# Optimization experiments

Hardware: AMD Instinct MI355X
Metric: run time of the kernel (lower is better)

## Reference

```python
import jax, jax.numpy as jnp
import numpy as np

R = 32          # grid_resolution
C_DIM = 128
HID = 128
N_BLOCKS = 5
PAD = 0.1
N_FREQ = 10

def setup_inputs() -> dict:
    key = jax.random.key(0)
    ks = jax.random.split(key, 10)
    B, T = 4, 65536
    s = 0.05
    return {
        "p": jax.random.uniform(ks[0], (B, T, 3), jnp.float32, -0.5, 0.5),
        "fc_pos_w": jax.random.normal(ks[1], (60, 2 * HID), jnp.float32) * s,
        "fc_pos_b": jax.random.normal(ks[2], (2 * HID,), jnp.float32) * s,
        "fc0_w": jax.random.normal(ks[3], (N_BLOCKS, 2 * HID, HID), jnp.float32) * s,
        "fc0_b": jax.random.normal(ks[4], (N_BLOCKS, HID), jnp.float32) * s,
        "fc1_w": jax.random.normal(ks[5], (N_BLOCKS, HID, HID), jnp.float32) * s,
        "fc1_b": jax.random.normal(ks[6], (N_BLOCKS, HID), jnp.float32) * s,
        "sc_w": jax.random.normal(ks[7], (N_BLOCKS, 2 * HID, HID), jnp.float32) * s,
        "fc_c_w": jax.random.normal(ks[8], (HID, C_DIM), jnp.float32) * s,
        "fc_c_b": jax.random.normal(ks[9], (C_DIM,), jnp.float32) * s,
    }

def _pos_enc(p):
    # NeRF-style: per frequency append sin then cos -> [B,T,3*2*10]=60
    freqs = (2.0 ** jnp.arange(N_FREQ, dtype=p.dtype)) * np.pi
    outs = []
    for i in range(N_FREQ):
        outs.append(jnp.sin(freqs[i] * p))
        outs.append(jnp.cos(freqs[i] * p))
    return jnp.concatenate(outs, axis=-1)

def _grid_index(p):
    # normalize_3d_coordinate + coordinate2index (3d)
    p_nor = p / (1.0 + PAD + 1e-3) + 0.5
    p_nor = jnp.clip(p_nor, 0.0, 1.0 - 1e-3)
    xi = (p_nor * R).astype(jnp.int32)
    return xi[..., 0] + R * (xi[..., 1] + R * xi[..., 2])  # [B,T]

def _resblock(x, w0, b0, w1, b1, ws):
    # ResnetBlockFC: fc_0(relu(x)) -> fc_1(relu(net)); shortcut Linear(no bias)
    net = jnp.maximum(x, 0) @ w0 + b0
    dx = jnp.maximum(net, 0) @ w1 + b1
    return x @ ws + dx

def _seg_max(c, idx):  # c [T,D], idx [T]
    return jax.ops.segment_max(c, idx, num_segments=R ** 3)

def _seg_sum(c, idx):
    return jax.ops.segment_sum(c, idx, num_segments=R ** 3)

def reference(p, fc_pos_w, fc_pos_b, fc0_w, fc0_b, fc1_w, fc1_b, sc_w, fc_c_w, fc_c_b):
    B = p.shape[0]
    index = _grid_index(p)                               # [B,T] int32
    net = _pos_enc(p) @ fc_pos_w + fc_pos_b              # [B,T,256]
    net = _resblock(net, fc0_w[0], fc0_b[0], fc1_w[0], fc1_b[0], sc_w[0])  # [B,T,128]
    for i in range(1, N_BLOCKS):
        # pool_local: scatter_max per voxel, gather back at each point
        fea = jax.vmap(_seg_max)(net, index)             # [B,R^3,128]
        pooled = jnp.take_along_axis(fea, index[..., None], axis=1)  # [B,T,128]
        net = jnp.concatenate([net, pooled], axis=-1)    # [B,T,256]
        net = _resblock(net, fc0_w[i], fc0_b[i], fc1_w[i], fc1_b[i], sc_w[i])
    c = net @ fc_c_w + fc_c_b                            # [B,T,128]
    # generate_grid_features: scatter_mean into R^3 voxels (empty voxels -> 0)
    sums = jax.vmap(_seg_sum)(c, index)                  # [B,R^3,128]
    cnt = jax.vmap(_seg_sum)(jnp.ones(index.shape + (1,), c.dtype), index)
    mean = sums / jnp.maximum(cnt, 1.0)
    fea_grid = mean.transpose(0, 2, 1).reshape(B, C_DIM, R, R, R)
    return fea_grid
```

## Files before the change

kernel.cpp:

```cpp
#include <hip/hip_runtime.h>

typedef _Float16 hf;
typedef _Float16 hf8 __attribute__((ext_vector_type(8)));
typedef float f32x4 __attribute__((ext_vector_type(4)));

static constexpr int BATCH = 4;
static constexpr int TPTS  = 65536;
static constexpr int NPTS  = BATCH * TPTS;
static constexpr int R3    = 32768;
static constexpr int NVOX  = BATCH * R3;

static constexpr int OFF_WPOS = 0;
static constexpr int OFF_W0   = 16384;
static constexpr int OFF_W1   = 180224;
static constexpr int OFF_WSC  = 262144;
static constexpr int OFF_WC   = 425984;
static constexpr int NCHUNKS  = 55296;

__device__ constexpr int kpat(int g, int j) { return (j & 3) + 4 * g + 16 * (j >> 2); }

#define MFMA16(a, b, c) __builtin_amdgcn_mfma_f32_16x16x32_f16((a), (b), (c), 0, 0, 0)

__device__ inline hf8 relu8(hf8 a) {
#pragma unroll
  for (int i = 0; i < 8; ++i) a[i] = (a[i] > (hf)0) ? a[i] : (hf)0;
  return a;
}
__device__ inline f32x4 splat4(float v) {
  f32x4 r; r[0] = v; r[1] = v; r[2] = v; r[3] = v; return r;
}
__device__ inline hf8 ldfrag(const hf* __restrict__ base, int kc, int nt, int NT, int lane) {
  return *(const hf8*)(base + (((size_t)(kc * NT + nt) * 64 + lane) << 3));
}

__global__ __launch_bounds__(256) void k_prep(
    const float* __restrict__ wpos, const float* __restrict__ w0,
    const float* __restrict__ w1,  const float* __restrict__ wsc,
    const float* __restrict__ wc,  hf* __restrict__ fr)
{
  const int cid = blockIdx.x * 256 + threadIdx.x;
  if (cid >= NCHUNKS) return;
  const float* src; hf* dst; int NT, N, kmax, loc;
  if (cid < 2048) {
    src = wpos; dst = fr + OFF_WPOS; NT = 16; N = 256; kmax = 60; loc = cid;
  } else if (cid < 22528) {
    int l5 = cid - 2048; int i = l5 >> 12; loc = l5 & 4095;
    src = w0 + (size_t)i * 32768; dst = fr + OFF_W0 + (size_t)i * 32768;
    NT = 8; N = 128; kmax = 256;
  } else if (cid < 32768) {
    int l5 = cid - 22528; int i = l5 >> 11; loc = l5 & 2047;
    src = w1 + (size_t)i * 16384; dst = fr + OFF_W1 + (size_t)i * 16384;
    NT = 8; N = 128; kmax = 128;
  } else if (cid < 53248) {
    int l5 = cid - 32768; int i = l5 >> 12; loc = l5 & 4095;
    src = wsc + (size_t)i * 32768; dst = fr + OFF_WSC + (size_t)i * 32768;
    NT = 8; N = 128; kmax = 256;
  } else {
    loc = cid - 53248; src = wc; dst = fr + OFF_WC; NT = 8; N = 128; kmax = 128;
  }
  const int lane = loc & 63;
  const int rest = loc >> 6;
  const int nt = rest % NT, kc = rest / NT;
  const int g = lane >> 4;
  const int n = nt * 16 + (lane & 15);
  union { hf8 h; hf f[8]; } o;
#pragma unroll
  for (int j = 0; j < 8; ++j) {
    int k = kc * 32 + kpat(g, j);
    o.f[j] = (k < kmax) ? (hf)src[(size_t)k * N + n] : (hf)0;
  }
  *(hf8*)(dst + ((size_t)loc << 3)) = o.h;
}

__global__ __launch_bounds__(256) void k_idxcnt(
    const float* __restrict__ p, int* __restrict__ idxbuf, int* __restrict__ cnt)
{
  const int t = blockIdx.x * 256 + threadIdx.x;
  const float px = p[(size_t)t * 3 + 0];
  const float py = p[(size_t)t * 3 + 1];
  const float pz = p[(size_t)t * 3 + 2];
  float nx = fminf(fmaxf(px / 1.101f + 0.5f, 0.0f), 0.999f);
  float ny = fminf(fmaxf(py / 1.101f + 0.5f, 0.0f), 0.999f);
  float nz = fminf(fmaxf(pz / 1.101f + 0.5f, 0.0f), 0.999f);
  const int iv = (int)(nx * 32.f) + 32 * (int)(ny * 32.f) + 1024 * (int)(nz * 32.f);
  idxbuf[t] = iv;
  atomicAdd(&cnt[((t >> 16) << 15) | iv], 1);
}

__global__ __launch_bounds__(256) void k_scan(
    const int* __restrict__ cnt, int* __restrict__ start, int* __restrict__ total)
{
  __shared__ int s[256];
  __shared__ int base_s;
  const int tid = threadIdx.x;
  const int v0 = blockIdx.x * 512;
  const int a = cnt[v0 + 2 * tid], b = cnt[v0 + 2 * tid + 1];
  const int sum = a + b;
  s[tid] = sum;
  __syncthreads();
  for (int off = 1; off < 256; off <<= 1) {
    int x = (tid >= off) ? s[tid - off] : 0;
    __syncthreads();
    s[tid] += x;
    __syncthreads();
  }
  if (tid == 255) base_s = atomicAdd(total, s[255]);
  __syncthreads();
  const int excl = base_s + s[tid] - sum;
  start[v0 + 2 * tid]     = excl;
  start[v0 + 2 * tid + 1] = excl + a;
}

__global__ __launch_bounds__(256) void k_fill(
    int* __restrict__ idxbuf, int* __restrict__ start, int* __restrict__ svox)
{
  const int t = blockIdx.x * 256 + threadIdx.x;
  const int bv = ((t >> 16) << 15) | idxbuf[t];
  const int pos = atomicAdd(&start[bv], 1);
  svox[pos] = bv;
  idxbuf[t] = pos;
}

__global__ __launch_bounds__(256, 4) void k_fused0(
    const float* __restrict__ p, const hf* __restrict__ fr,
    const float* __restrict__ bpos,
    const hf* __restrict__ w0f, const hf* __restrict__ w1f,
    const hf* __restrict__ wscf,
    const float* __restrict__ b0, const float* __restrict__ b1,
    const int* __restrict__ spos, hf* __restrict__ net)
{
  __shared__ __align__(16) hf swX[16384];
  __shared__ int sp[64];
  const int tid = threadIdx.x;
  const int wv = tid >> 6, lane = tid & 63;
  const int r = lane & 15, g = lane >> 4;
  const int t0 = blockIdx.x * 64;

  if (tid < 64) sp[tid] = spos[t0 + tid];

  if (tid < 64) {
    const int mt = tid >> 4, rr = tid & 15;
    *(unsigned long long*)(swX + (((mt * 2 + 1) * 64 + 48 + rr) << 3) + 4) = 0ull;
  }
#pragma unroll
  for (int i = 0; i < 8; ++i) {
    const int tau = tid + i * 256;
    if (tau >= 1920) break;
    const int pt = (int)(((unsigned)tau * 34953u) >> 20);
    const int a  = tau - pt * 30;
    const int fi = (a * 11) >> 5;
    const int comp = a - 3 * fi;
    const float pc = p[(size_t)(t0 + pt) * 3 + comp];
    const float ang = (float)(1 << fi) * 3.14159274101257324f * pc;
    const float sv = __sinf(ang), cv = __cosf(ang);
    const int mt = pt >> 4, rr = pt & 15;
    const int ks = 6 * fi + comp;
    {
      const int kc = ks >> 5, kk = ks & 31, gg = (kk >> 2) & 3;
      const int e = (kk & 3) + 4 * (kk >> 4);
      swX[(((mt * 2 + kc) * 64 + gg * 16 + rr) << 3) + e] = (hf)sv;
    }
    {
      const int kco = ks + 3;
      const int kc = kco >> 5, kk = kco & 31, gg = (kk >> 2) & 3;
      const int e = (kk & 3) + 4 * (kk >> 4);
      swX[(((mt * 2 + kc) * 64 + gg * 16 + rr) << 3) + e] = (hf)cv;
    }
  }
  __syncthreads();

  f32x4 acc[4][4];
#pragma unroll
  for (int nf = 0; nf < 4; ++nf) {
    float bv = bpos[wv * 64 + nf * 16 + r];
#pragma unroll
    for (int mf = 0; mf < 4; ++mf) acc[mf][nf] = splat4(bv);
  }
#pragma unroll
  for (int kc = 0; kc < 2; ++kc) {
    hf8 a[4];
#pragma unroll
    for (int mf = 0; mf < 4; ++mf)
      a[mf] = *(const hf8*)(swX + (((mf * 2 + kc) * 64 + lane) << 3));
#pragma unroll
    for (int nf = 0; nf < 4; ++nf) {
      hf8 b = ldfrag(fr + OFF_WPOS, kc, wv * 4 + nf, 16, lane);
#pragma unroll
      for (int mf = 0; mf < 4; ++mf) acc[mf][nf] = MFMA16(a[mf], b, acc[mf][nf]);
    }
  }
  __syncthreads();

#pragma unroll
  for (int mf = 0; mf < 4; ++mf)
#pragma unroll
    for (int nf = 0; nf < 4; ++nf)
#pragma unroll
      for (int reg = 0; reg < 4; ++reg) {
        int rr = 4 * g + reg;
        int c  = wv * 64 + nf * 16 + r;
        int kc = c >> 5;
        int kk = c & 31;
        int gg = (kk >> 2) & 3;
        int e  = (kk & 3) + 4 * (kk >> 4);
        int slot = gg * 16 + ((rr + gg) & 15);
        swX[(((size_t)(mf * 8 + kc) * 64 + slot) << 3) + e] = (hf)acc[mf][nf][reg];
      }
  __syncthreads();

  const int wm = wv >> 1, wn = wv & 1;
  const int lidx = g * 16 + ((r + g) & 15);

  f32x4 h[2][4], d[2][4];
#pragma unroll
  for (int nf = 0; nf < 4; ++nf) {
    const int n = wn * 64 + nf * 16 + r;
    const float bh = b0[n], bd = b1[n];
#pragma unroll
    for (int mf = 0; mf < 2; ++mf) { h[mf][nf] = splat4(bh); d[mf][nf] = splat4(bd); }
  }
#pragma unroll 2
  for (int kc = 0; kc < 8; ++kc) {
    hf8 a[2], ar[2];
#pragma unroll
    for (int mf = 0; mf < 2; ++mf) {
      a[mf] = *(const hf8*)(swX + (((size_t)((wm * 2 + mf) * 8 + kc) * 64 + lidx) << 3));
      ar[mf] = relu8(a[mf]);
    }
#pragma unroll
    for (int nf = 0; nf < 4; ++nf) {
      hf8 bw0 = ldfrag(w0f, kc, wn * 4 + nf, 8, lane);
      hf8 bws = ldfrag(wscf, kc, wn * 4 + nf, 8, lane);
#pragma unroll
      for (int mf = 0; mf < 2; ++mf) {
        h[mf][nf] = MFMA16(ar[mf], bw0, h[mf][nf]);
        d[mf][nf] = MFMA16(a[mf],  bws, d[mf][nf]);
      }
    }
  }
  __syncthreads();

#pragma unroll
  for (int mf = 0; mf < 2; ++mf)
#pragma unroll
    for (int nf = 0; nf < 4; ++nf)
#pragma unroll
      for (int reg = 0; reg < 4; ++reg) {
        int m = wm * 32 + mf * 16 + 4 * g + reg;
        int k = wn * 64 + nf * 16 + r;
        float hv = fmaxf(h[mf][nf][reg], 0.f);
        int mt = m >> 4, rr = m & 15;
        int kc = k >> 5, kk = k & 31;
        int gg = (kk >> 2) & 3;
        int e = (kk & 3) + 4 * (kk >> 4);
        int slot = gg * 16 + ((rr + gg) & 15);
        swX[(((size_t)(mt * 4 + kc) * 64 + slot) << 3) + e] = (hf)hv;
      }
  __syncthreads();

#pragma unroll
  for (int kc = 0; kc < 4; ++kc) {
    hf8 a[2];
#pragma unroll
    for (int mf = 0; mf < 2; ++mf)
      a[mf] = *(const hf8*)(swX + (((size_t)((wm * 2 + mf) * 4 + kc) * 64 + lidx) << 3));
#pragma unroll
    for (int nf = 0; nf < 4; ++nf) {
      hf8 bw1 = ldfrag(w1f, kc, wn * 4 + nf, 8, lane);
#pragma unroll
      for (int mf = 0; mf < 2; ++mf) d[mf][nf] = MFMA16(a[mf], bw1, d[mf][nf]);
    }
  }

#pragma unroll
  for (int mf = 0; mf < 2; ++mf)
#pragma unroll
    for (int nf = 0; nf < 4; ++nf)
#pragma unroll
      for (int reg = 0; reg < 4; ++reg) {
        int m = wm * 32 + mf * 16 + 4 * g + reg;
        int n = wn * 64 + nf * 16 + r;
        net[(size_t)sp[m] * 128 + n] = (hf)d[mf][nf][reg];
      }
}

__global__ __launch_bounds__(256) void k_pool(
    const hf* __restrict__ net, const int* __restrict__ svox,
    hf* __restrict__ fea)
{
  const int tid = threadIdx.x;
  const int grp = tid >> 4, q = tid & 15;
  const int gbeg = blockIdx.x * 128 + grp * 8;
  const int gend = gbeg + 8;
  int i = gbeg;
  while (i < gend) {
    const int v = svox[i];
    if (i != 0 && svox[i - 1] == v) { ++i; continue; }
    float m[8];
#pragma unroll
    for (int e = 0; e < 8; ++e) m[e] = -1e30f;
    int j = i;
    do {
      union { uint4 u; hf h[8]; } x;
      x.u = *(const uint4*)(net + (size_t)j * 128 + 8 * q);
#pragma unroll
      for (int e = 0; e < 8; ++e) m[e] = fmaxf(m[e], (float)x.h[e]);
      ++j;
    } while (j < NPTS && svox[j] == v);
    union { uint4 u; hf h[8]; } o;
#pragma unroll
    for (int e = 0; e < 8; ++e) o.h[e] = (hf)m[e];
    *(uint4*)(fea + ((size_t)v << 7) + 8 * q) = o.u;
    i = j;
  }
}

template <int LAST>
__global__ __launch_bounds__(256, 2) void k_res(
    hf* __restrict__ net, const hf* __restrict__ fea,
    const int* __restrict__ svox,
    const hf* __restrict__ w0f, const hf* __restrict__ w1f,
    const hf* __restrict__ wscf,
    const float* __restrict__ b0, const float* __restrict__ b1,
    const hf* __restrict__ wcf, const float* __restrict__ bc)
{
  __shared__ __align__(16) hf swX[32768];
  const int tid = threadIdx.x;
  const int wv = tid >> 6, lane = tid & 63;
  const int r = lane & 15, g = lane >> 4;
  const int wm = wv >> 1, wn = wv & 1;
  const int t0 = blockIdx.x * 128;
  const int lidx = g * 16 + ((r + g) & 15);

  for (int cc = tid; cc < 4096; cc += 256) {
    const int cl = cc & 63;
    const int kc = (cc >> 6) & 7;
    const int mt = cc >> 9;
    const int rr = cl & 15, gg = cl >> 4;
    const int t = t0 + mt * 16 + rr;
    const int c1 = kc * 32 + 4 * gg;
    union { hf8 h; uint2 u2[2]; } x;
    const hf* srcp;
    if (kc < 4) {
      srcp = net + (size_t)t * 128 + c1;
    } else {
      srcp = fea + (((size_t)svox[t]) << 7) + (c1 - 128);
    }
    x.u2[0] = *(const uint2*)(srcp);
    x.u2[1] = *(const uint2*)(srcp + 16);
    const int slot = gg * 16 + ((rr + gg) & 15);
    *(hf8*)(swX + (((size_t)((cc & ~63) + slot)) << 3)) = x.h;
  }
  __syncthreads();

  f32x4 h[4][4], d[4][4];
#pragma unroll
  for (int nf = 0; nf < 4; ++nf) {
    const int n = wn * 64 + nf * 16 + r;
    const float bh = b0[n], bd = b1[n];
#pragma unroll
    for (int mf = 0; mf < 4; ++mf) { h[mf][nf] = splat4(bh); d[mf][nf] = splat4(bd); }
  }
#pragma unroll 2
  for (int kc = 0; kc < 8; ++kc) {
    hf8 a[4], ar[4];
#pragma unroll
    for (int mf = 0; mf < 4; ++mf) {
      a[mf] = *(const hf8*)(swX + (((size_t)((wm * 4 + mf) * 8 + kc) * 64 + lidx) << 3));
      ar[mf] = relu8(a[mf]);
    }
#pragma unroll
    for (int nf = 0; nf < 4; ++nf) {
      hf8 bw0 = ldfrag(w0f, kc, wn * 4 + nf, 8, lane);
      hf8 bws = ldfrag(wscf, kc, wn * 4 + nf, 8, lane);
#pragma unroll
      for (int mf = 0; mf < 4; ++mf) {
        h[mf][nf] = MFMA16(ar[mf], bw0, h[mf][nf]);
        d[mf][nf] = MFMA16(a[mf],  bws, d[mf][nf]);
      }
    }
  }
  __syncthreads();

#pragma unroll
  for (int mf = 0; mf < 4; ++mf)
#pragma unroll
    for (int nf = 0; nf < 4; ++nf)
#pragma unroll
      for (int reg = 0; reg < 4; ++reg) {
        int m = wm * 64 + mf * 16 + 4 * g + reg;
        int k = wn * 64 + nf * 16 + r;
        float hv = fmaxf(h[mf][nf][reg], 0.f);
        int mt = m >> 4, rr = m & 15;
        int kc = k >> 5, kk = k & 31;
        int gg = (kk >> 2) & 3;
        int e = (kk & 3) + 4 * (kk >> 4);
        int slot = gg * 16 + ((rr + gg) & 15);
        swX[(((size_t)(mt * 4 + kc) * 64 + slot) << 3) + e] = (hf)hv;
      }
  __syncthreads();

#pragma unroll
  for (int kc = 0; kc < 4; ++kc) {
    hf8 a[4];
#pragma unroll
    for (int mf = 0; mf < 4; ++mf)
      a[mf] = *(const hf8*)(swX + (((size_t)((wm * 4 + mf) * 4 + kc) * 64 + lidx) << 3));
#pragma unroll
    for (int nf = 0; nf < 4; ++nf) {
      hf8 bw1 = ldfrag(w1f, kc, wn * 4 + nf, 8, lane);
#pragma unroll
      for (int mf = 0; mf < 4; ++mf) d[mf][nf] = MFMA16(a[mf], bw1, d[mf][nf]);
    }
  }

  if (LAST) {
    __syncthreads();
#pragma unroll
    for (int mf = 0; mf < 4; ++mf)
#pragma unroll
      for (int nf = 0; nf < 4; ++nf)
#pragma unroll
        for (int reg = 0; reg < 4; ++reg) {
          int m = wm * 64 + mf * 16 + 4 * g + reg;
          int k = wn * 64 + nf * 16 + r;
          int mt = m >> 4, rr = m & 15;
          int kc = k >> 5, kk = k & 31;
          int gg = (kk >> 2) & 3;
          int e = (kk & 3) + 4 * (kk >> 4);
          int slot = gg * 16 + ((rr + gg) & 15);
          swX[(((size_t)(mt * 4 + kc) * 64 + slot) << 3) + e] = (hf)d[mf][nf][reg];
        }
    __syncthreads();

    f32x4 c2[4][4];
#pragma unroll
    for (int nf = 0; nf < 4; ++nf) {
      float bv = bc[wn * 64 + nf * 16 + r];
#pragma unroll
      for (int mf = 0; mf < 4; ++mf) c2[mf][nf] = splat4(bv);
    }
#pragma unroll
    for (int kc = 0; kc < 4; ++kc) {
      hf8 a[4];
#pragma unroll
      for (int mf = 0; mf < 4; ++mf)
        a[mf] = *(const hf8*)(swX + (((size_t)((wm * 4 + mf) * 4 + kc) * 64 + lidx) << 3));
#pragma unroll
      for (int nf = 0; nf < 4; ++nf) {
        hf8 bw = ldfrag(wcf, kc, wn * 4 + nf, 8, lane);
#pragma unroll
        for (int mf = 0; mf < 4; ++mf) c2[mf][nf] = MFMA16(a[mf], bw, c2[mf][nf]);
      }
    }
#pragma unroll
    for (int mf = 0; mf < 4; ++mf)
#pragma unroll
      for (int nf = 0; nf < 4; ++nf)
#pragma unroll
        for (int reg = 0; reg < 4; ++reg) {
          int m = wm * 64 + mf * 16 + 4 * g + reg;
          int n = wn * 64 + nf * 16 + r;
          net[(size_t)(t0 + m) * 128 + n] = (hf)c2[mf][nf][reg];
        }
  } else {
#pragma unroll
    for (int mf = 0; mf < 4; ++mf)
#pragma unroll
      for (int nf = 0; nf < 4; ++nf)
#pragma unroll
        for (int reg = 0; reg < 4; ++reg) {
          int m = wm * 64 + mf * 16 + 4 * g + reg;
          int n = wn * 64 + nf * 16 + r;
          net[(size_t)(t0 + m) * 128 + n] = (hf)d[mf][nf][reg];
        }
  }
}

__global__ __launch_bounds__(256) void k_write(
    const hf* __restrict__ cbuf, const int* __restrict__ start,
    const int* __restrict__ cnt, float* __restrict__ out)
{
  __shared__ float tile[128 * 65];
  const int tid = threadIdx.x;
  const int grp = tid >> 4, q = tid & 15;
  const int g0 = blockIdx.x * 64;
  for (int vl = grp; vl < 64; vl += 16) {
    const int bv = g0 + vl;
    const int n = cnt[bv];
    const int end = start[bv], beg = end - n;
    float s[8] = {0, 0, 0, 0, 0, 0, 0, 0};
    for (int i = beg; i < end; ++i) {
      union { uint4 u; hf h[8]; } x;
      x.u = *(const uint4*)(cbuf + (size_t)i * 128 + 8 * q);
#pragma unroll
      for (int e = 0; e < 8; ++e) s[e] += (float)x.h[e];
    }
    const float inv = 1.0f / fmaxf((float)n, 1.0f);
#pragma unroll
    for (int e = 0; e < 8; ++e) tile[(8 * q + e) * 65 + vl] = s[e] * inv;
  }
  __syncthreads();
  const int b = g0 >> 15, v0 = g0 & 32767;
  for (int i = tid; i < 8192; i += 256) {
    const int c = i >> 6, vl = i & 63;
    out[(((size_t)(b * 128 + c)) << 15) + v0 + vl] = tile[c * 65 + vl];
  }
}

extern "C" void kernel_launch(void* const* d_in, const int* in_sizes, int n_in,
                              void* d_out, int out_size, void* d_ws, size_t ws_size,
                              hipStream_t stream)
{
  const float* p    = (const float*)d_in[0];
  const float* wpos = (const float*)d_in[1];
  const float* bpos = (const float*)d_in[2];
  const float* w0   = (const float*)d_in[3];
  const float* b0   = (const float*)d_in[4];
  const float* w1   = (const float*)d_in[5];
  const float* b1   = (const float*)d_in[6];
  const float* wsc  = (const float*)d_in[7];
  const float* wc   = (const float*)d_in[8];
  const float* bc   = (const float*)d_in[9];

  char* ws = (char*)d_ws;
  int* idxbuf = (int*)ws;
  hf*  net    = (hf*)(ws + (1u << 20));
  hf*  fea    = (hf*)(ws + (65u << 20));
  int* cnt32  = (int*)(ws + (97u << 20));
  int* total  = (int*)(ws + (97u << 20) + 0x80000);
  int* startb = (int*)(ws + (97u << 20) + 0x80400);
  int* svox   = (int*)(ws + (97u << 20) + 0x100400);
  hf*  fr     = (hf*)d_out;

  k_prep<<<216, 256, 0, stream>>>(wpos, w0, w1, wsc, wc, fr);

  hipMemsetAsync(cnt32, 0, 0x80000 + 0x400, stream);
  k_idxcnt<<<NPTS / 256, 256, 0, stream>>>(p, idxbuf, cnt32);
  k_scan<<<NVOX / 512, 256, 0, stream>>>(cnt32, startb, total);
  k_fill<<<NPTS / 256, 256, 0, stream>>>(idxbuf, startb, svox);

  k_fused0<<<NPTS / 64, 256, 0, stream>>>(p, fr, bpos,
      fr + OFF_W0, fr + OFF_W1, fr + OFF_WSC, b0, b1, idxbuf, net);

  for (int i = 1; i < 4; ++i) {
    k_pool<<<NPTS / 128, 256, 0, stream>>>(net, svox, fea);
    k_res<0><<<NPTS / 128, 256, 0, stream>>>(net, fea, svox,
        fr + OFF_W0 + (size_t)i * 32768, fr + OFF_W1 + (size_t)i * 16384,
        fr + OFF_WSC + (size_t)i * 32768, b0 + i * 128, b1 + i * 128,
        nullptr, nullptr);
  }
  k_pool<<<NPTS / 128, 256, 0, stream>>>(net, svox, fea);
  k_res<1><<<NPTS / 128, 256, 0, stream>>>(net, fea, svox,
      fr + OFF_W0 + (size_t)4 * 32768, fr + OFF_W1 + (size_t)4 * 16384,
      fr + OFF_WSC + (size_t)4 * 32768, b0 + 4 * 128, b1 + 4 * 128,
      fr + OFF_WC, bc);

  k_write<<<NVOX / 64, 256, 0, stream>>>(net, startb, cnt32, (float*)d_out);
}
```

Measured before the change: 619.2 us.

## Fuse voxel max-pool into residual block kernel with ping-pong net buffers

When the workspace is large enough, the separate pooling kernel is removed. Each residual block now computes the per-voxel max directly from the sorted point list (svox/startb/cnt) while staging its tile into LDS. It reads from one net buffer and writes to the other, which avoids the hazard of pooling while writing in place. This removes a kernel launch and the fea write/read round-trip per block. The cost is redundant max recomputation when a tile's voxels span many points, and scalar LDS writes with divergent loops.

```diff
diff --git a/kernel.cpp b/kernel.cpp
--- a/kernel.cpp
+++ b/kernel.cpp
@@ -315,10 +315,11 @@
   }
 }
 
-template <int LAST>
+template <int LAST, int POOLIN>
 __global__ __launch_bounds__(256, 2) void k_res(
-    hf* __restrict__ net, const hf* __restrict__ fea,
-    const int* __restrict__ svox,
+    const hf* __restrict__ netin, hf* __restrict__ netout,
+    const hf* __restrict__ fea, const int* __restrict__ svox,
+    const int* __restrict__ startb, const int* __restrict__ cnt,
     const hf* __restrict__ w0f, const hf* __restrict__ w1f,
     const hf* __restrict__ wscf,
     const float* __restrict__ b0, const float* __restrict__ b1,
@@ -332,24 +333,77 @@
   const int t0 = blockIdx.x * 128;
   const int lidx = g * 16 + ((r + g) & 15);
 
-  for (int cc = tid; cc < 4096; cc += 256) {
-    const int cl = cc & 63;
-    const int kc = (cc >> 6) & 7;
-    const int mt = cc >> 9;
-    const int rr = cl & 15, gg = cl >> 4;
-    const int t = t0 + mt * 16 + rr;
-    const int c1 = kc * 32 + 4 * gg;
-    union { hf8 h; uint2 u2[2]; } x;
-    const hf* srcp;
-    if (kc < 4) {
-      srcp = net + (size_t)t * 128 + c1;
-    } else {
-      srcp = fea + (((size_t)svox[t]) << 7) + (c1 - 128);
-    }
-    x.u2[0] = *(const uint2*)(srcp);
-    x.u2[1] = *(const uint2*)(srcp + 16);
-    const int slot = gg * 16 + ((rr + gg) & 15);
-    *(hf8*)(swX + (((size_t)((cc & ~63) + slot)) << 3)) = x.h;
+  if (POOLIN) {
+    for (int cc = tid; cc < 2048; cc += 256) {
+      const int cl = cc & 63;
+      const int kc = (cc >> 6) & 3;
+      const int mt = cc >> 8;
+      const int rr = cl & 15, gg = cl >> 4;
+      const int t = t0 + mt * 16 + rr;
+      const int c1 = kc * 32 + 4 * gg;
+      union { hf8 h; uint2 u2[2]; } x;
+      const hf* srcp = netin + (size_t)t * 128 + c1;
+      x.u2[0] = *(const uint2*)(srcp);
+      x.u2[1] = *(const uint2*)(srcp + 16);
+      const int slot = gg * 16 + ((rr + gg) & 15);
+      *(hf8*)(swX + (((size_t)((mt * 8 + kc) * 64 + slot)) << 3)) = x.h;
+    }
+    {
+      const int grp = tid >> 4, q = tid & 15;
+      const int rbase = t0 + grp * 8;
+      int vprev = -1;
+      float m[8];
+#pragma unroll
+      for (int e = 0; e < 8; ++e) m[e] = -1e30f;
+      for (int rloc = 0; rloc < 8; ++rloc) {
+        const int t = rbase + rloc;
+        const int v = svox[t];
+        if (v != vprev) {
+          vprev = v;
+          const int end = startb[v];
+          const int beg = end - cnt[v];
+#pragma unroll
+          for (int e = 0; e < 8; ++e) m[e] = -1e30f;
+          for (int j = beg; j < end; ++j) {
+            union { uint4 u; hf h[8]; } x;
+            x.u = *(const uint4*)(netin + (size_t)j * 128 + 8 * q);
+#pragma unroll
+            for (int e = 0; e < 8; ++e) m[e] = fmaxf(m[e], (float)x.h[e]);
+          }
+        }
+        const int mt = (t - t0) >> 4, rr = (t - t0) & 15;
+#pragma unroll
+        for (int i = 0; i < 8; ++i) {
+          const int c = 128 + 8 * q + i;
+          const int kc = c >> 5;
+          const int kk = c & 31;
+          const int gg = (kk >> 2) & 3;
+          const int e = (kk & 3) + 4 * (kk >> 4);
+          const int slot = gg * 16 + ((rr + gg) & 15);
+          swX[(((size_t)((mt * 8 + kc) * 64 + slot)) << 3) + e] = (hf)m[i];
+        }
+      }
+    }
+  } else {
+    for (int cc = tid; cc < 4096; cc += 256) {
+      const int cl = cc & 63;
+      const int kc = (cc >> 6) & 7;
+      const int mt = cc >> 9;
+      const int rr = cl & 15, gg = cl >> 4;
+      const int t = t0 + mt * 16 + rr;
+      const int c1 = kc * 32 + 4 * gg;
+      union { hf8 h; uint2 u2[2]; } x;
+      const hf* srcp;
+      if (kc < 4) {
+        srcp = netin + (size_t)t * 128 + c1;
+      } else {
+        srcp = fea + (((size_t)svox[t]) << 7) + (c1 - 128);
+      }
+      x.u2[0] = *(const uint2*)(srcp);
+      x.u2[1] = *(const uint2*)(srcp + 16);
+      const int slot = gg * 16 + ((rr + gg) & 15);
+      *(hf8*)(swX + (((size_t)((cc & ~63) + slot)) << 3)) = x.h;
+    }
   }
   __syncthreads();
 
@@ -461,7 +515,7 @@
         for (int reg = 0; reg < 4; ++reg) {
           int m = wm * 64 + mf * 16 + 4 * g + reg;
           int n = wn * 64 + nf * 16 + r;
-          net[(size_t)(t0 + m) * 128 + n] = (hf)c2[mf][nf][reg];
+          netout[(size_t)(t0 + m) * 128 + n] = (hf)c2[mf][nf][reg];
         }
   } else {
 #pragma unroll
@@ -472,7 +526,7 @@
         for (int reg = 0; reg < 4; ++reg) {
           int m = wm * 64 + mf * 16 + 4 * g + reg;
           int n = wn * 64 + nf * 16 + r;
-          net[(size_t)(t0 + m) * 128 + n] = (hf)d[mf][nf][reg];
+          netout[(size_t)(t0 + m) * 128 + n] = (hf)d[mf][nf][reg];
         }
   }
 }
@@ -524,14 +578,38 @@
   const float* bc   = (const float*)d_in[9];
 
   char* ws = (char*)d_ws;
-  int* idxbuf = (int*)ws;
-  hf*  net    = (hf*)(ws + (1u << 20));
-  hf*  fea    = (hf*)(ws + (65u << 20));
-  int* cnt32  = (int*)(ws + (97u << 20));
-  int* total  = (int*)(ws + (97u << 20) + 0x80000);
-  int* startb = (int*)(ws + (97u << 20) + 0x80400);
-  int* svox   = (int*)(ws + (97u << 20) + 0x100400);
-  hf*  fr     = (hf*)d_out;
+  hf*  fr  = (hf*)d_out;
+
+  const size_t OFF_IDX  = 0;
+  const size_t OFF_NETA = (size_t)1u << 20;
+  const size_t OFF_NETB = (size_t)65u << 20;
+  const size_t OFF_CNT  = (size_t)129u << 20;
+  const size_t OFF_TOT  = OFF_CNT + 0x80000;
+  const size_t OFF_STR  = OFF_CNT + 0x80400;
+  const size_t OFF_SVX  = OFF_CNT + 0x100400;
+  const size_t NEED     = OFF_SVX + ((size_t)1u << 20);
+  const bool big = (ws_size >= NEED);
+
+  int* idxbuf; hf* netA; hf* netB; hf* fea; int* cnt32; int* total; int* startb; int* svox;
+  if (big) {
+    idxbuf = (int*)(ws + OFF_IDX);
+    netA   = (hf*)(ws + OFF_NETA);
+    netB   = (hf*)(ws + OFF_NETB);
+    fea    = nullptr;
+    cnt32  = (int*)(ws + OFF_CNT);
+    total  = (int*)(ws + OFF_TOT);
+    startb = (int*)(ws + OFF_STR);
+    svox   = (int*)(ws + OFF_SVX);
+  } else {
+    idxbuf = (int*)ws;
+    netA   = (hf*)(ws + (1u << 20));
+    netB   = netA;
+    fea    = (hf*)(ws + (65u << 20));
+    cnt32  = (int*)(ws + (97u << 20));
+    total  = (int*)(ws + (97u << 20) + 0x80000);
+    startb = (int*)(ws + (97u << 20) + 0x80400);
+    svox   = (int*)(ws + (97u << 20) + 0x100400);
+  }
 
   k_prep<<<216, 256, 0, stream>>>(wpos, w0, w1, wsc, wc, fr);
 
@@ -541,20 +619,38 @@
   k_fill<<<NPTS / 256, 256, 0, stream>>>(idxbuf, startb, svox);
 
   k_fused0<<<NPTS / 64, 256, 0, stream>>>(p, fr, bpos,
-      fr + OFF_W0, fr + OFF_W1, fr + OFF_WSC, b0, b1, idxbuf, net);
-
-  for (int i = 1; i < 4; ++i) {
-    k_pool<<<NPTS / 128, 256, 0, stream>>>(net, svox, fea);
-    k_res<0><<<NPTS / 128, 256, 0, stream>>>(net, fea, svox,
-        fr + OFF_W0 + (size_t)i * 32768, fr + OFF_W1 + (size_t)i * 16384,
-        fr + OFF_WSC + (size_t)i * 32768, b0 + i * 128, b1 + i * 128,
-        nullptr, nullptr);
-  }
-  k_pool<<<NPTS / 128, 256, 0, stream>>>(net, svox, fea);
-  k_res<1><<<NPTS / 128, 256, 0, stream>>>(net, fea, svox,
-      fr + OFF_W0 + (size_t)4 * 32768, fr + OFF_W1 + (size_t)4 * 16384,
-      fr + OFF_WSC + (size_t)4 * 32768, b0 + 4 * 128, b1 + 4 * 128,
-      fr + OFF_WC, bc);
-
-  k_write<<<NVOX / 64, 256, 0, stream>>>(net, startb, cnt32, (float*)d_out);
-}
+      fr + OFF_W0, fr + OFF_W1, fr + OFF_WSC, b0, b1, idxbuf, netA);
+
+  if (big) {
+    hf* bufs[2] = { netA, netB };
+    for (int i = 1; i < 4; ++i) {
+      k_res<0, 1><<<NPTS / 128, 256, 0, stream>>>(
+          bufs[(i + 1) & 1], bufs[i & 1], nullptr, svox, startb, cnt32,
+          fr + OFF_W0 + (size_t)i * 32768, fr + OFF_W1 + (size_t)i * 16384,
+          fr + OFF_WSC + (size_t)i * 32768, b0 + i * 128, b1 + i * 128,
+          nullptr, nullptr);
+    }
+    k_res<1, 1><<<NPTS / 128, 256, 0, stream>>>(
+        netB, netA, nullptr, svox, startb, cnt32,
+        fr + OFF_W0 + (size_t)4 * 32768, fr + OFF_W1 + (size_t)4 * 16384,
+        fr + OFF_WSC + (size_t)4 * 32768, b0 + 4 * 128, b1 + 4 * 128,
+        fr + OFF_WC, bc);
+  } else {
+    for (int i = 1; i < 4; ++i) {
+      k_pool<<<NPTS / 128, 256, 0, stream>>>(netA, svox, fea);
+      k_res<0, 0><<<NPTS / 128, 256, 0, stream>>>(
+          netA, netA, fea, svox, startb, cnt32,
+          fr + OFF_W0 + (size_t)i * 32768, fr + OFF_W1 + (size_t)i * 16384,
+          fr + OFF_WSC + (size_t)i * 32768, b0 + i * 128, b1 + i * 128,
+          nullptr, nullptr);
+    }
+    k_pool<<<NPTS / 128, 256, 0, stream>>>(netA, svox, fea);
+    k_res<1, 0><<<NPTS / 128, 256, 0, stream>>>(
+        netA, netA, fea, svox, startb, cnt32,
+        fr + OFF_W0 + (size_t)4 * 32768, fr + OFF_W1 + (size_t)4 * 16384,
+        fr + OFF_WSC + (size_t)4 * 32768, b0 + 4 * 128, b1 + 4 * 128,
+        fr + OFF_WC, bc);
+  }
+
+  k_write<<<NVOX / 64, 256, 0, stream>>>(netA, startb, cnt32, (float*)d_out);
+}
```

Result: faster. 566.4 us (-8.5%).

## Fuse voxel max-pooling into resblock kernel with ping-pong net buffers

Applied to the files above, without the earlier changes.

Removes the separate k_pool launch and the fea intermediate buffer. Each k_res block now computes the per-voxel max for its own points directly from the sorted input net, using start/count offsets, and writes the pooled half into shared memory between the two K-halves of the first GEMM. Because other blocks must read the old net while this block writes, net is double-buffered. Shared memory is halved so occupancy can rise to 4 blocks per CU. The trade-off is redundant voxel-max work at block boundaries and an extra barrier stage.

```diff
diff --git a/kernel.cpp b/kernel.cpp
--- a/kernel.cpp
+++ b/kernel.cpp
@@ -284,47 +284,17 @@
       }
 }
 
-__global__ __launch_bounds__(256) void k_pool(
-    const hf* __restrict__ net, const int* __restrict__ svox,
-    hf* __restrict__ fea)
-{
-  const int tid = threadIdx.x;
-  const int grp = tid >> 4, q = tid & 15;
-  const int gbeg = blockIdx.x * 128 + grp * 8;
-  const int gend = gbeg + 8;
-  int i = gbeg;
-  while (i < gend) {
-    const int v = svox[i];
-    if (i != 0 && svox[i - 1] == v) { ++i; continue; }
-    float m[8];
-#pragma unroll
-    for (int e = 0; e < 8; ++e) m[e] = -1e30f;
-    int j = i;
-    do {
-      union { uint4 u; hf h[8]; } x;
-      x.u = *(const uint4*)(net + (size_t)j * 128 + 8 * q);
-#pragma unroll
-      for (int e = 0; e < 8; ++e) m[e] = fmaxf(m[e], (float)x.h[e]);
-      ++j;
-    } while (j < NPTS && svox[j] == v);
-    union { uint4 u; hf h[8]; } o;
-#pragma unroll
-    for (int e = 0; e < 8; ++e) o.h[e] = (hf)m[e];
-    *(uint4*)(fea + ((size_t)v << 7) + 8 * q) = o.u;
-    i = j;
-  }
-}
-
 template <int LAST>
-__global__ __launch_bounds__(256, 2) void k_res(
-    hf* __restrict__ net, const hf* __restrict__ fea,
+__global__ __launch_bounds__(256, 4) void k_res(
+    const hf* __restrict__ netin, hf* __restrict__ netout,
     const int* __restrict__ svox,
+    const int* __restrict__ startb, const int* __restrict__ cnt,
     const hf* __restrict__ w0f, const hf* __restrict__ w1f,
     const hf* __restrict__ wscf,
     const float* __restrict__ b0, const float* __restrict__ b1,
     const hf* __restrict__ wcf, const float* __restrict__ bc)
 {
-  __shared__ __align__(16) hf swX[32768];
+  __shared__ __align__(16) hf swX[16384];
   const int tid = threadIdx.x;
   const int wv = tid >> 6, lane = tid & 63;
   const int r = lane & 15, g = lane >> 4;
@@ -332,26 +302,20 @@
   const int t0 = blockIdx.x * 128;
   const int lidx = g * 16 + ((r + g) & 15);
 
-  for (int cc = tid; cc < 4096; cc += 256) {
+  for (int cc = tid; cc < 2048; cc += 256) {
     const int cl = cc & 63;
-    const int kc = (cc >> 6) & 7;
-    const int mt = cc >> 9;
+    const int kc = (cc >> 6) & 3;
+    const int mt = cc >> 8;
     const int rr = cl & 15, gg = cl >> 4;
     const int t = t0 + mt * 16 + rr;
     const int c1 = kc * 32 + 4 * gg;
     union { hf8 h; uint2 u2[2]; } x;
-    const hf* srcp;
-    if (kc < 4) {
-      srcp = net + (size_t)t * 128 + c1;
-    } else {
-      srcp = fea + (((size_t)svox[t]) << 7) + (c1 - 128);
-    }
+    const hf* srcp = netin + (size_t)t * 128 + c1;
     x.u2[0] = *(const uint2*)(srcp);
     x.u2[1] = *(const uint2*)(srcp + 16);
     const int slot = gg * 16 + ((rr + gg) & 15);
-    *(hf8*)(swX + (((size_t)((cc & ~63) + slot)) << 3)) = x.h;
-  }
-  __syncthreads();
+    *(hf8*)(swX + (((size_t)((mt * 4 + kc) * 64 + slot)) << 3)) = x.h;
+  }
 
   f32x4 h[4][4], d[4][4];
 #pragma unroll
@@ -361,12 +325,75 @@
 #pragma unroll
     for (int mf = 0; mf < 4; ++mf) { h[mf][nf] = splat4(bh); d[mf][nf] = splat4(bd); }
   }
+  __syncthreads();
+
 #pragma unroll 2
-  for (int kc = 0; kc < 8; ++kc) {
+  for (int kc = 0; kc < 4; ++kc) {
     hf8 a[4], ar[4];
 #pragma unroll
     for (int mf = 0; mf < 4; ++mf) {
-      a[mf] = *(const hf8*)(swX + (((size_t)((wm * 4 + mf) * 8 + kc) * 64 + lidx) << 3));
+      a[mf] = *(const hf8*)(swX + (((size_t)((wm * 4 + mf) * 4 + kc) * 64 + lidx) << 3));
+      ar[mf] = relu8(a[mf]);
+    }
+#pragma unroll
+    for (int nf = 0; nf < 4; ++nf) {
+      hf8 bw0 = ldfrag(w0f, kc, wn * 4 + nf, 8, lane);
+      hf8 bws = ldfrag(wscf, kc, wn * 4 + nf, 8, lane);
+#pragma unroll
+      for (int mf = 0; mf < 4; ++mf) {
+        h[mf][nf] = MFMA16(ar[mf], bw0, h[mf][nf]);
+        d[mf][nf] = MFMA16(a[mf],  bws, d[mf][nf]);
+      }
+    }
+  }
+  __syncthreads();
+
+  {
+    const int grp = tid >> 4, q = tid & 15;
+    const int q3 = q & 3;
+    const int kcp = q >> 2;
+    const int hi = q3 >> 1;
+    const int rbase = t0 + grp * 8;
+    int vprev = -1;
+    float m[8];
+#pragma unroll
+    for (int e = 0; e < 8; ++e) m[e] = -1e30f;
+    for (int rloc = 0; rloc < 8; ++rloc) {
+      const int t = rbase + rloc;
+      const int v = svox[t];
+      if (v != vprev) {
+        vprev = v;
+        const int end = startb[v];
+        const int beg = end - cnt[v];
+#pragma unroll
+        for (int e = 0; e < 8; ++e) m[e] = -1e30f;
+        for (int j = beg; j < end; ++j) {
+          union { uint4 u; hf hh[8]; } x;
+          x.u = *(const uint4*)(netin + (size_t)j * 128 + 8 * q);
+#pragma unroll
+          for (int e = 0; e < 8; ++e) m[e] = fmaxf(m[e], (float)x.hh[e]);
+        }
+      }
+      const int mt = (t - t0) >> 4, rr = (t - t0) & 15;
+#pragma unroll
+      for (int j = 0; j < 2; ++j) {
+        const int gg = (2 * q3 + j) & 3;
+        const int slot = gg * 16 + ((rr + gg) & 15);
+        union { unsigned long long u; hf f[4]; } pk;
+#pragma unroll
+        for (int ii = 0; ii < 4; ++ii) pk.f[ii] = (hf)m[4 * j + ii];
+        *(unsigned long long*)(swX + (((size_t)((mt * 4 + kcp) * 64 + slot)) << 3) + 4 * hi) = pk.u;
+      }
+    }
+  }
+  __syncthreads();
+
+#pragma unroll 2
+  for (int kc = 4; kc < 8; ++kc) {
+    hf8 a[4], ar[4];
+#pragma unroll
+    for (int mf = 0; mf < 4; ++mf) {
+      a[mf] = *(const hf8*)(swX + (((size_t)((wm * 4 + mf) * 4 + (kc - 4)) * 64 + lidx) << 3));
       ar[mf] = relu8(a[mf]);
     }
 #pragma unroll
@@ -461,7 +488,7 @@
         for (int reg = 0; reg < 4; ++reg) {
           int m = wm * 64 + mf * 16 + 4 * g + reg;
           int n = wn * 64 + nf * 16 + r;
-          net[(size_t)(t0 + m) * 128 + n] = (hf)c2[mf][nf][reg];
+          netout[(size_t)(t0 + m) * 128 + n] = (hf)c2[mf][nf][reg];
         }
   } else {
 #pragma unroll
@@ -472,7 +499,7 @@
         for (int reg = 0; reg < 4; ++reg) {
           int m = wm * 64 + mf * 16 + 4 * g + reg;
           int n = wn * 64 + nf * 16 + r;
-          net[(size_t)(t0 + m) * 128 + n] = (hf)d[mf][nf][reg];
+          netout[(size_t)(t0 + m) * 128 + n] = (hf)d[mf][nf][reg];
         }
   }
 }
@@ -524,37 +551,39 @@
   const float* bc   = (const float*)d_in[9];
 
   char* ws = (char*)d_ws;
+  hf*  fr  = (hf*)d_out;
+
   int* idxbuf = (int*)ws;
-  hf*  net    = (hf*)(ws + (1u << 20));
-  hf*  fea    = (hf*)(ws + (65u << 20));
-  int* cnt32  = (int*)(ws + (97u << 20));
-  int* total  = (int*)(ws + (97u << 20) + 0x80000);
-  int* startb = (int*)(ws + (97u << 20) + 0x80400);
-  int* svox   = (int*)(ws + (97u << 20) + 0x100400);
-  hf*  fr     = (hf*)d_out;
+  hf*  netA   = (hf*)(ws + ((size_t)1u << 20));
+  hf*  netB   = (hf*)(ws + ((size_t)65u << 20));
+  int* cnt32  = (int*)(ws + ((size_t)129u << 20));
+  int* startb = (int*)(ws + ((size_t)129u << 20) + 0x80400);
+  int* svox   = (int*)(ws + ((size_t)129u << 20) + 0x100400);
 
   k_prep<<<216, 256, 0, stream>>>(wpos, w0, w1, wsc, wc, fr);
 
   hipMemsetAsync(cnt32, 0, 0x80000 + 0x400, stream);
   k_idxcnt<<<NPTS / 256, 256, 0, stream>>>(p, idxbuf, cnt32);
-  k_scan<<<NVOX / 512, 256, 0, stream>>>(cnt32, startb, total);
+  k_scan<<<NVOX / 512, 256, 0, stream>>>(cnt32, startb,
+                                         (int*)(ws + ((size_t)129u << 20) + 0x80000));
   k_fill<<<NPTS / 256, 256, 0, stream>>>(idxbuf, startb, svox);
 
   k_fused0<<<NPTS / 64, 256, 0, stream>>>(p, fr, bpos,
-      fr + OFF_W0, fr + OFF_W1, fr + OFF_WSC, b0, b1, idxbuf, net);
-
+      fr + OFF_W0, fr + OFF_W1, fr + OFF_WSC, b0, b1, idxbuf, netA);
+
+  hf* bufs[2] = { netA, netB };
   for (int i = 1; i < 4; ++i) {
-    k_pool<<<NPTS / 128, 256, 0, stream>>>(net, svox, fea);
-    k_res<0><<<NPTS / 128, 256, 0, stream>>>(net, fea, svox,
+    k_res<0><<<NPTS / 128, 256, 0, stream>>>(
+        bufs[(i + 1) & 1], bufs[i & 1], svox, startb, cnt32,
         fr + OFF_W0 + (size_t)i * 32768, fr + OFF_W1 + (size_t)i * 16384,
         fr + OFF_WSC + (size_t)i * 32768, b0 + i * 128, b1 + i * 128,
         nullptr, nullptr);
   }
-  k_pool<<<NPTS / 128, 256, 0, stream>>>(net, svox, fea);
-  k_res<1><<<NPTS / 128, 256, 0, stream>>>(net, fea, svox,
+  k_res<1><<<NPTS / 128, 256, 0, stream>>>(
+      netB, netA, svox, startb, cnt32,
       fr + OFF_W0 + (size_t)4 * 32768, fr + OFF_W1 + (size_t)4 * 16384,
       fr + OFF_WSC + (size_t)4 * 32768, b0 + 4 * 128, b1 + 4 * 128,
       fr + OFF_WC, bc);
 
-  k_write<<<NVOX / 64, 256, 0, stream>>>(net, startb, cnt32, (float*)d_out);
-}
+  k_write<<<NVOX / 64, 256, 0, stream>>>(netA, startb, cnt32, (float*)d_out);
+}
```

After: 1.968 ms. 218% more time.
